# Optimization experiments

Measured on AMD Instinct MI355X. Metric: run time of the kernel, lower is better.

Reference implementation:

```python
import jax, jax.numpy as jnp
import numpy as np

B, T = 32, 512
LATENT, COND, HIDDEN, OUT, E = 64, 448, 1024, 512, 8
INPUT = LATENT + COND            # 512
INTER = LATENT + COND + HIDDEN   # 1536
GATE_H = 64


def setup_inputs() -> dict:
    key = jax.random.key(0)
    ks = jax.random.split(key, 20)
    d = {
        "z": jax.random.normal(ks[0], (B, T, LATENT), dtype=jnp.float32),
        "c": jax.random.normal(ks[1], (B, T, COND), dtype=jnp.float32),
    }
    # expert weights: kaiming-uniform-ish init, biases filled with 0.01 (as in torch code)
    layer_dims = [(INPUT, HIDDEN), (INTER, HIDDEN), (INTER, HIDDEN), (INTER, HIDDEN), (INTER, OUT)]
    for i, (fin, fout) in enumerate(layer_dims):
        bound = float(np.sqrt(6.0 / fin))
        d[f"w{i}"] = jax.random.uniform(ks[2 + i], (E, fin, fout), dtype=jnp.float32, minval=-bound, maxval=bound)
        d[f"b{i}"] = jnp.full((E, fout), 0.01, dtype=jnp.float32)
    # gate MLP: input_size -> 64 -> 64 -> E (stored as [in, out])
    gate_dims = [(INPUT, GATE_H), (GATE_H, GATE_H), (GATE_H, E)]
    for i, (fin, fout) in enumerate(gate_dims):
        bound = float(np.sqrt(1.0 / fin))
        d[f"gw{i}"] = jax.random.uniform(ks[10 + 2 * i], (fin, fout), dtype=jnp.float32, minval=-bound, maxval=bound)
        d[f"gb{i}"] = jax.random.uniform(ks[11 + 2 * i], (fout,), dtype=jnp.float32, minval=-bound, maxval=bound)
    return d


def reference(z, c, w0, b0, w1, b1, w2, b2, w3, b3, w4, b4, gw0, gb0, gw1, gb1, gw2, gb2):
    # gate -> per-token softmax mixing coefficients  [B, T, E]
    x = jnp.concatenate([z, c], axis=-1)
    h = jax.nn.leaky_relu(x @ gw0 + gb0)
    h = jax.nn.leaky_relu(h @ gw1 + gb1)
    coef = jax.nn.softmax(h @ gw2 + gb2, axis=-1)
    # Original computes mixed_weight for every t but baddbmm uses only mixed_weight[:, 0];
    # so the effective per-sequence weight uses coefficients at t=0 only (same math, no huge intermediate).
    coef0 = coef[:, 0]  # [B, E]
    layer_out = c
    layers = [(w0, b0, True), (w1, b1, True), (w2, b2, True), (w3, b3, True), (w4, b4, False)]
    for i, (w, b, act) in enumerate(layers):
        if i == 0:
            inp = jnp.concatenate([z, layer_out], axis=-1)      # [B, T, INPUT]
        else:
            inp = jnp.concatenate([z, c, layer_out], axis=-1)   # [B, T, INTER]
        wm = jnp.einsum('be,eio->bio', coef0, w)                # per-sequence mixed weight
        bm = jnp.einsum('bte,eo->bto', coef, b)                 # per-token mixed bias
        out = bm + jnp.einsum('bti,bio->bto', inp, wm)
        layer_out = jax.nn.leaky_relu(out) if act else out
    return layer_out
```

## Files before the change

### kernel.cpp

```cpp
#include <hip/hip_runtime.h>
#include <math.h>

#define B_     32
#define T_     512
#define LATENT 64
#define COND   448
#define HIDDEN 1024
#define OUTD   512
#define E_     8
#define INPUT_ 512
#define INTER_ 1536
#define GATEH  64
#define NTOK   (B_ * T_)
#define KTAIL  32

typedef __attribute__((ext_vector_type(8))) short short8;
typedef __attribute__((ext_vector_type(4))) float f32x4;

static __device__ __forceinline__ unsigned short f2bf(float x) {
    unsigned u = __float_as_uint(x);
    u += 0x7fffu + ((u >> 16) & 1u);
    return (unsigned short)(u >> 16);
}

__global__ __launch_bounds__(256) void wprep_kernel(
    const float* __restrict__ gw0, const float* __restrict__ gw1,
    unsigned short* __restrict__ gw0T, unsigned short* __restrict__ gw1T)
{
    int idx = blockIdx.x * 256 + threadIdx.x;
    if (idx < GATEH * INPUT_) {
        int n = idx >> 9, k = idx & 511;
        gw0T[n * INPUT_ + k] = f2bf(gw0[k * GATEH + n]);
    } else {
        int i2 = idx - GATEH * INPUT_;
        if (i2 < GATEH * GATEH) {
            int n = i2 >> 6, k = i2 & 63;
            gw1T[n * GATEH + k] = f2bf(gw1[k * GATEH + n]);
        }
    }
}

__global__ __launch_bounds__(256) void gate_kernel(
    const float* __restrict__ z, const float* __restrict__ c,
    const float* __restrict__ gb0,
    const float* __restrict__ gb1,
    const float* __restrict__ gw2, const float* __restrict__ gb2,
    const unsigned short* __restrict__ gw0T,
    const unsigned short* __restrict__ gw1T,
    float* __restrict__ coef, unsigned short* __restrict__ coefpad,
    unsigned short* __restrict__ xzb)
{
    __shared__ unsigned short Hb[GATEH][72];
    __shared__ float H2[GATEH][65];
    __shared__ float sLg[GATEH][E_];

    const int tid = threadIdx.x;
    const int lane = tid & 63;
    const int wv = tid >> 6;
    const int tok0 = blockIdx.x * 64;

#pragma unroll
    for (int i = 0; i < 4; ++i) {
        int idx = i * 256 + tid;
        int tr = idx >> 4, c4 = (idx & 15) * 4;
        float4 v = *(const float4*)(z + ((size_t)(tok0 + tr) * LATENT) + c4);
        ushort4 o = {f2bf(v.x), f2bf(v.y), f2bf(v.z), f2bf(v.w)};
        *(ushort4*)(xzb + (size_t)(tok0 + tr) * INPUT_ + c4) = o;
    }
#pragma unroll
    for (int i = 0; i < 28; ++i) {
        int idx = i * 256 + tid;
        int tr = idx / 112, c4 = (idx % 112) * 4;
        float4 v = *(const float4*)(c + ((size_t)(tok0 + tr) * COND) + c4);
        ushort4 o = {f2bf(v.x), f2bf(v.y), f2bf(v.z), f2bf(v.w)};
        *(ushort4*)(xzb + (size_t)(tok0 + tr) * INPUT_ + LATENT + c4) = o;
    }
    __threadfence_block();
    __syncthreads();

    const int fr = lane & 15, fq = lane >> 4;
    const int wm0 = (wv & 1) * 32, wn0 = (wv >> 1) * 32;

    f32x4 acc[2][2];
#pragma unroll
    for (int im = 0; im < 2; ++im)
#pragma unroll
        for (int in = 0; in < 2; ++in) acc[im][in] = (f32x4){0.f,0.f,0.f,0.f};

    for (int k0 = 0; k0 < INPUT_; k0 += 32) {
        short8 af[2], bf[2];
#pragma unroll
        for (int im = 0; im < 2; ++im)
            af[im] = *(const short8*)(xzb + (size_t)(tok0 + wm0 + im*16 + fr) * INPUT_
                                          + k0 + fq * 8);
#pragma unroll
        for (int in = 0; in < 2; ++in)
            bf[in] = *(const short8*)(gw0T + (size_t)(wn0 + in*16 + fr) * INPUT_
                                           + k0 + fq * 8);
#pragma unroll
        for (int im = 0; im < 2; ++im)
#pragma unroll
            for (int in = 0; in < 2; ++in)
                acc[im][in] = __builtin_amdgcn_mfma_f32_16x16x32_bf16(
                    af[im], bf[in], acc[im][in], 0, 0, 0);
    }
#pragma unroll
    for (int im = 0; im < 2; ++im)
#pragma unroll
        for (int in = 0; in < 2; ++in)
#pragma unroll
            for (int reg = 0; reg < 4; ++reg) {
                int m = wm0 + im*16 + fq*4 + reg;
                int n = wn0 + in*16 + fr;
                float h = acc[im][in][reg] + gb0[n];
                h = h > 0.f ? h : 0.01f * h;
                Hb[m][n] = f2bf(h);
            }
    __syncthreads();

    f32x4 a2[2][2];
#pragma unroll
    for (int im = 0; im < 2; ++im)
#pragma unroll
        for (int in = 0; in < 2; ++in) a2[im][in] = (f32x4){0.f,0.f,0.f,0.f};
#pragma unroll
    for (int k0 = 0; k0 < GATEH; k0 += 32) {
        short8 af[2], bf[2];
#pragma unroll
        for (int im = 0; im < 2; ++im)
            af[im] = *(const short8*)(&Hb[wm0 + im*16 + fr][k0 + fq*8]);
#pragma unroll
        for (int in = 0; in < 2; ++in)
            bf[in] = *(const short8*)(gw1T + (size_t)(wn0 + in*16 + fr) * GATEH
                                           + k0 + fq * 8);
#pragma unroll
        for (int im = 0; im < 2; ++im)
#pragma unroll
            for (int in = 0; in < 2; ++in)
                a2[im][in] = __builtin_amdgcn_mfma_f32_16x16x32_bf16(
                    af[im], bf[in], a2[im][in], 0, 0, 0);
    }
#pragma unroll
    for (int im = 0; im < 2; ++im)
#pragma unroll
        for (int in = 0; in < 2; ++in)
#pragma unroll
            for (int reg = 0; reg < 4; ++reg) {
                int m = wm0 + im*16 + fq*4 + reg;
                int n = wn0 + in*16 + fr;
                float h = a2[im][in][reg] + gb1[n];
                H2[m][n] = h > 0.f ? h : 0.01f * h;
            }
    __syncthreads();

    {
        int tok = tid >> 2, e0 = (tid & 3) * 2;
        float l0 = gb2[e0], l1 = gb2[e0 + 1];
#pragma unroll
        for (int i = 0; i < GATEH; ++i) {
            float h = H2[tok][i];
            l0 = fmaf(h, gw2[i * E_ + e0], l0);
            l1 = fmaf(h, gw2[i * E_ + e0 + 1], l1);
        }
        sLg[tok][e0] = l0; sLg[tok][e0 + 1] = l1;
    }
    __syncthreads();

    if (tid < 64) {
        int token = tok0 + tid;
        float lg[E_], m = -1e30f, s = 0.f;
#pragma unroll
        for (int e = 0; e < E_; ++e) { lg[e] = sLg[tid][e]; m = fmaxf(m, lg[e]); }
#pragma unroll
        for (int e = 0; e < E_; ++e) { lg[e] = expf(lg[e] - m); s += lg[e]; }
        float inv = 1.f / s;
        unsigned short pad[KTAIL];
#pragma unroll
        for (int e = 0; e < E_; ++e) {
            float cv = lg[e] * inv;
            coef[(size_t)token * E_ + e] = cv;
            pad[e] = f2bf(cv);
        }
#pragma unroll
        for (int j = E_; j < KTAIL; ++j) pad[j] = 0;
#pragma unroll
        for (int q = 0; q < 4; ++q)
            *(ushort4*)(coefpad + (size_t)token * KTAIL + q * 4) =
                *(const ushort4*)&pad[q * 4];
    }
}

#define MI 32
#define MO 64
#define MP 65

__global__ __launch_bounds__(256) void mixT_kernel(
    const float* __restrict__ w,
    const float* __restrict__ bias,
    const float* __restrict__ coef,
    unsigned short* __restrict__ wmT,
    int fin, int fout, int gb, int batch0)
{
    __shared__ float sW[E_][MI][MP];
    __shared__ float sC[B_][E_];
    const int t = threadIdx.x;
    const int fin_tot = fin + KTAIL;
    const int nbi = fin / MI;
    const int i0 = (blockIdx.x % nbi) * MI;
    const int o0 = (blockIdx.x / nbi) * MO;

    if (t < gb * E_)
        sC[t >> 3][t & 7] = coef[(size_t)(batch0 + (t >> 3)) * T_ * E_ + (t & 7)];

#pragma unroll
    for (int r = 0; r < 64; ++r) {
        int idx = r * 256 + t;
        int o = idx & 63;
        int i = (idx >> 6) & 31;
        int e = idx >> 11;
        sW[e][i][o] = w[(size_t)e * fin * fout + (size_t)(i0 + i) * fout + o0 + o];
    }
    __syncthreads();

    const int o  = t >> 2;
    const int i8 = (t & 3) * 8;
    for (int b = 0; b < gb; ++b) {
        float v[8];
#pragma unroll
        for (int j = 0; j < 8; ++j) v[j] = 0.f;
#pragma unroll
        for (int e = 0; e < E_; ++e) {
            float cc = sC[b][e];
#pragma unroll
            for (int j = 0; j < 8; ++j)
                v[j] = fmaf(cc, sW[e][i8 + j][o], v[j]);
        }
        unsigned short u[8];
#pragma unroll
        for (int j = 0; j < 8; ++j) u[j] = f2bf(v[j]);
        *(int4*)(wmT + ((size_t)b * fout + o0 + o) * fin_tot + i0 + i8) = *(const int4*)u;
    }

    if (i0 == 0) {
        const int jj = t & 3;
        unsigned short u[8];
#pragma unroll
        for (int q = 0; q < 8; ++q)
            u[q] = (jj == 0) ? f2bf(bias[(size_t)q * fout + o0 + o]) : 0;
        for (int b = 0; b < gb; ++b)
            *(int4*)(wmT + ((size_t)b * fout + o0 + o) * fin_tot + fin + jj * 8) =
                *(const int4*)u;
    }
}

__global__ __launch_bounds__(512, 2) void gemm_kernel(
    const unsigned short* __restrict__ xz,
    const unsigned short* __restrict__ prev,
    const unsigned short* __restrict__ wmT,
    const unsigned short* __restrict__ coefpad,
    float* __restrict__ outf,
    unsigned short* __restrict__ outb,
    int fin_tot, int fout, int act, int batch0)
{
    __shared__ __align__(16) unsigned short As[4][8192];
    __shared__ __align__(16) unsigned short Bs[4][8192];

    const int tid = threadIdx.x;
    const int lane = tid & 63;
    const int w8 = tid >> 6;
    const int wm = w8 & 1;
    const int wn = w8 >> 1;

    const int nx = gridDim.x;
    int bx = blockIdx.x, by = blockIdx.y, bz = blockIdx.z;
    {
        int nwg = nx * 2 * gridDim.z;
        if ((nwg & 7) == 0) {
            int f = blockIdx.x + nx * (blockIdx.y + 2 * blockIdx.z);
            int q = nwg >> 3;
            int wk = (f & 7) * q + (f >> 3);
            int bpb = nx * 2;
            bz = wk / bpb;
            int r = wk - bz * bpb;
            by = r / nx;
            bx = r - by * nx;
        }
    }

    const int row0 = by * 256;
    const int col0 = bx * 256;
    const size_t tokbase = (size_t)(batch0 + bz) * T_;
    const unsigned short* wmb = wmT + (size_t)bz * fin_tot * fout;

    const int lrow = lane >> 2;
    const int lk8  = (((lane & 3) ^ ((lane >> 3) & 3)) * 8);
    const int fr = lane & 15, fq = lane >> 4;
    const int koff = (fq ^ ((fr >> 1) & 3)) * 8;
    const int ktail0 = fin_tot - KTAIL;
    const int nt = fin_tot >> 5;

    f32x4 acc[8][4];
#pragma unroll
    for (int im = 0; im < 8; ++im)
#pragma unroll
        for (int in = 0; in < 4; ++in)
            acc[im][in] = (f32x4){0.f, 0.f, 0.f, 0.f};

    auto stage = [&](int t) {
        int k0 = t << 5;
        const unsigned short* abase; int astr, acol;
        if (k0 < INPUT_)      { abase = xz;      astr = INPUT_; acol = k0; }
        else if (k0 < ktail0) { abase = prev;    astr = HIDDEN; acol = k0 - INPUT_; }
        else                  { abase = coefpad; astr = KTAIL;  acol = 0; }
        unsigned short* Ab = As[t & 3];
        unsigned short* Bb = Bs[t & 3];
#pragma unroll
        for (int j = 0; j < 2; ++j) {
            int ch = w8 + 8 * j;
            const unsigned short* srcA = abase
                + (tokbase + row0 + ch * 16 + lrow) * (size_t)astr + acol + lk8;
            __builtin_amdgcn_global_load_lds(
                (const __attribute__((address_space(1))) unsigned int*)(const void*)srcA,
                (__attribute__((address_space(3))) unsigned int*)(void*)(Ab + ch * 512),
                16, 0, 0);
            const unsigned short* srcB = wmb
                + (size_t)(col0 + ch * 16 + lrow) * fin_tot + k0 + lk8;
            __builtin_amdgcn_global_load_lds(
                (const __attribute__((address_space(1))) unsigned int*)(const void*)srcB,
                (__attribute__((address_space(3))) unsigned int*)(void*)(Bb + ch * 512),
                16, 0, 0);
        }
    };

    stage(0);
    if (nt > 1) stage(1);
    if (nt > 2) stage(2);

    for (int t = 0; t < nt; ++t) {
        int rem = nt - 1 - t;
        if (rem >= 2)
            asm volatile("s_waitcnt vmcnt(8)\n\ts_barrier" ::: "memory");
        else if (rem == 1)
            asm volatile("s_waitcnt vmcnt(4)\n\ts_barrier" ::: "memory");
        else
            asm volatile("s_waitcnt vmcnt(0)\n\ts_barrier" ::: "memory");

        if (t + 3 < nt) stage(t + 3);

        const unsigned short* Ab = As[t & 3] + wm * 4096;
        const unsigned short* Bb = Bs[t & 3] + wn * 2048;
        short8 af[8], bfv[4];
#pragma unroll
        for (int im = 0; im < 8; ++im)
            af[im] = *(const short8*)(Ab + im * 512 + fr * 32 + koff);
#pragma unroll
        for (int in = 0; in < 4; ++in)
            bfv[in] = *(const short8*)(Bb + in * 512 + fr * 32 + koff);

        __builtin_amdgcn_s_setprio(1);
#pragma unroll
        for (int im = 0; im < 8; ++im)
#pragma unroll
            for (int in = 0; in < 4; ++in)
                acc[im][in] = __builtin_amdgcn_mfma_f32_16x16x32_bf16(
                    af[im], bfv[in], acc[im][in], 0, 0, 0);
        __builtin_amdgcn_s_setprio(0);
    }

#pragma unroll
    for (int im = 0; im < 8; ++im) {
#pragma unroll
        for (int in = 0; in < 4; ++in) {
#pragma unroll
            for (int reg = 0; reg < 4; ++reg) {
                int r = wm * 128 + im * 16 + fq * 4 + reg;
                int col = wn * 64 + in * 16 + fr;
                float v = acc[im][in][reg];
                if (act) v = v > 0.f ? v : 0.01f * v;
                size_t off = (tokbase + row0 + r) * fout + col0 + col;
                if (outb) outb[off] = f2bf(v);
                else      outf[off] = v;
            }
        }
    }
}

extern "C" void kernel_launch(void* const* d_in, const int* in_sizes, int n_in,
                              void* d_out, int out_size, void* d_ws, size_t ws_size,
                              hipStream_t stream)
{
    const float* z = (const float*)d_in[0];
    const float* c = (const float*)d_in[1];
    const float* w[5]  = {(const float*)d_in[2], (const float*)d_in[4],
                          (const float*)d_in[6], (const float*)d_in[8],
                          (const float*)d_in[10]};
    const float* bs[5] = {(const float*)d_in[3], (const float*)d_in[5],
                          (const float*)d_in[7], (const float*)d_in[9],
                          (const float*)d_in[11]};
    const float* gw0 = (const float*)d_in[12]; const float* gb0 = (const float*)d_in[13];
    const float* gw1 = (const float*)d_in[14]; const float* gb1 = (const float*)d_in[15];
    const float* gw2 = (const float*)d_in[16]; const float* gb2 = (const float*)d_in[17];

    const size_t g0t_b  = (size_t)GATEH * INPUT_ * 2;
    const size_t g1t_b  = (size_t)GATEH * GATEH * 2;
    const size_t xz_b   = (size_t)NTOK * INPUT_ * 2;
    const size_t coef_b = (size_t)NTOK * E_ * 4;
    const size_t cpad_b = (size_t)NTOK * KTAIL * 2;
    const size_t act_b  = (size_t)NTOK * HIDDEN * 2;
    const size_t wmun   = (size_t)(INTER_ + KTAIL) * HIDDEN * 2;

    char* p = (char*)d_ws;
    unsigned short* gw0T  = (unsigned short*)p;  p += g0t_b;
    unsigned short* gw1T  = (unsigned short*)p;  p += g1t_b;
    unsigned short* xzb   = (unsigned short*)p;  p += xz_b;
    float*          coef  = (float*)p;           p += coef_b;
    unsigned short* cpad  = (unsigned short*)p;  p += cpad_b;
    unsigned short* actB  = (unsigned short*)p;  p += act_b;

    size_t base = g0t_b + g1t_b + xz_b + coef_b + cpad_b + act_b;
    size_t avail = (ws_size > base) ? ws_size - base : 0;

    int gb;
    unsigned short* actA;
    unsigned short* wmT;
    if (avail >= act_b + 32 * wmun) {
        gb = 32; actA = (unsigned short*)p; p += act_b; wmT = (unsigned short*)p;
    } else {
        actA = (unsigned short*)d_out;
        wmT  = (unsigned short*)p;
        gb = 1;
        for (int g = 16; g >= 2; g >>= 1)
            if (avail >= (size_t)g * wmun) { gb = g; break; }
    }

    wprep_kernel<<<(GATEH * (INPUT_ + GATEH) + 255) / 256, 256, 0, stream>>>(
        gw0, gw1, gw0T, gw1T);
    gate_kernel<<<NTOK / 64, 256, 0, stream>>>(
        z, c, gb0, gb1, gw2, gb2, gw0T, gw1T, coef, cpad, xzb);

    struct L { int fin, fout, act; const unsigned short* in; unsigned short* outb; };
    L Ls[5] = {
        {INPUT_, HIDDEN, 1, actB , actA},
        {INTER_, HIDDEN, 1, actA, actB},
        {INTER_, HIDDEN, 1, actB, actA},
        {INTER_, HIDDEN, 1, actA, actB},
        {INTER_, OUTD,   0, actB, 0},
    };

    for (int Li = 0; Li < 5; ++Li) {
        int fin = Ls[Li].fin, fout = Ls[Li].fout;
        int nblk = (fin / MI) * (fout / MO);
        for (int g = 0; g < B_; g += gb) {
            mixT_kernel<<<nblk, 256, 0, stream>>>(
                w[Li], bs[Li], coef, wmT, fin, fout, gb, g);
            gemm_kernel<<<dim3(fout / 256, T_ / 256, gb), 512, 0, stream>>>(
                xzb, Ls[Li].in, wmT, cpad,
                (float*)d_out, Ls[Li].outb, fin + KTAIL, fout, Ls[Li].act, g);
        }
    }
}
```

Measured before the change: 698.4 us.

## Restructure GEMM main loop into BK=64 ping-pong schedule with interleaved staging

Doubles the K step per iteration to 64, switching from a 4-deep ring of 32-wide stages to a double-buffered pair of 64-wide stages. Each iteration is split into four quarter-phases that interleave global-to-LDS loads for the next tile with LDS reads and MFMA clusters, separated by barriers. The coefficient/bias tail is padded to 64 columns so K stays a multiple of 64, adding extra zero K work and more barriers. The aim is better overlap of memory and MFMA with fewer outer iterations, at the cost of a shallower prefetch depth.

```diff
diff --git a/kernel.cpp b/kernel.cpp
--- a/kernel.cpp
+++ b/kernel.cpp
@@ -12,7 +12,7 @@
 #define INTER_ 1536
 #define GATEH  64
 #define NTOK   (B_ * T_)
-#define KTAIL  32
+#define KTAIL  64
 
 typedef __attribute__((ext_vector_type(8))) short short8;
 typedef __attribute__((ext_vector_type(4))) float f32x4;
@@ -184,7 +184,7 @@
 #pragma unroll
         for (int j = E_; j < KTAIL; ++j) pad[j] = 0;
 #pragma unroll
-        for (int q = 0; q < 4; ++q)
+        for (int q = 0; q < KTAIL / 4; ++q)
             *(ushort4*)(coefpad + (size_t)token * KTAIL + q * 4) =
                 *(const ushort4*)&pad[q * 4];
     }
@@ -247,9 +247,12 @@
 #pragma unroll
         for (int q = 0; q < 8; ++q)
             u[q] = (jj == 0) ? f2bf(bias[(size_t)q * fout + o0 + o]) : 0;
-        for (int b = 0; b < gb; ++b)
-            *(int4*)(wmT + ((size_t)b * fout + o0 + o) * fin_tot + fin + jj * 8) =
-                *(const int4*)u;
+        unsigned short z8[8] = {0, 0, 0, 0, 0, 0, 0, 0};
+        for (int b = 0; b < gb; ++b) {
+            size_t rb = ((size_t)b * fout + o0 + o) * fin_tot + fin;
+            *(int4*)(wmT + rb + jj * 8)      = *(const int4*)u;
+            *(int4*)(wmT + rb + 32 + jj * 8) = *(const int4*)z8;
+        }
     }
 }
 
@@ -262,8 +265,8 @@
     unsigned short* __restrict__ outb,
     int fin_tot, int fout, int act, int batch0)
 {
-    __shared__ __align__(16) unsigned short As[4][8192];
-    __shared__ __align__(16) unsigned short Bs[4][8192];
+    __shared__ __align__(16) unsigned short As[2][2][8192];
+    __shared__ __align__(16) unsigned short Bs[2][2][8192];
 
     const int tid = threadIdx.x;
     const int lane = tid & 63;
@@ -297,7 +300,7 @@
     const int fr = lane & 15, fq = lane >> 4;
     const int koff = (fq ^ ((fr >> 1) & 3)) * 8;
     const int ktail0 = fin_tot - KTAIL;
-    const int nt = fin_tot >> 5;
+    const int nt = fin_tot >> 6;
 
     f32x4 acc[8][4];
 #pragma unroll
@@ -306,64 +309,144 @@
         for (int in = 0; in < 4; ++in)
             acc[im][in] = (f32x4){0.f, 0.f, 0.f, 0.f};
 
-    auto stage = [&](int t) {
-        int k0 = t << 5;
+    auto stageA = [&](int t, int kk) {
+        int k32 = (t << 6) + (kk << 5);
         const unsigned short* abase; int astr, acol;
-        if (k0 < INPUT_)      { abase = xz;      astr = INPUT_; acol = k0; }
-        else if (k0 < ktail0) { abase = prev;    astr = HIDDEN; acol = k0 - INPUT_; }
-        else                  { abase = coefpad; astr = KTAIL;  acol = 0; }
-        unsigned short* Ab = As[t & 3];
-        unsigned short* Bb = Bs[t & 3];
+        if (k32 < INPUT_)      { abase = xz;      astr = INPUT_; acol = k32; }
+        else if (k32 < ktail0) { abase = prev;    astr = HIDDEN; acol = k32 - INPUT_; }
+        else                   { abase = coefpad; astr = KTAIL;  acol = k32 - ktail0; }
+        unsigned short* Ab = &As[t & 1][kk][0];
 #pragma unroll
         for (int j = 0; j < 2; ++j) {
             int ch = w8 + 8 * j;
-            const unsigned short* srcA = abase
+            const unsigned short* src = abase
                 + (tokbase + row0 + ch * 16 + lrow) * (size_t)astr + acol + lk8;
             __builtin_amdgcn_global_load_lds(
-                (const __attribute__((address_space(1))) unsigned int*)(const void*)srcA,
+                (const __attribute__((address_space(1))) unsigned int*)(const void*)src,
                 (__attribute__((address_space(3))) unsigned int*)(void*)(Ab + ch * 512),
                 16, 0, 0);
-            const unsigned short* srcB = wmb
-                + (size_t)(col0 + ch * 16 + lrow) * fin_tot + k0 + lk8;
+        }
+    };
+    auto stageB = [&](int t, int kk) {
+        int k32 = (t << 6) + (kk << 5);
+        unsigned short* Bb = &Bs[t & 1][kk][0];
+#pragma unroll
+        for (int j = 0; j < 2; ++j) {
+            int ch = w8 + 8 * j;
+            const unsigned short* src = wmb
+                + (size_t)(col0 + ch * 16 + lrow) * fin_tot + k32 + lk8;
             __builtin_amdgcn_global_load_lds(
-                (const __attribute__((address_space(1))) unsigned int*)(const void*)srcB,
+                (const __attribute__((address_space(1))) unsigned int*)(const void*)src,
                 (__attribute__((address_space(3))) unsigned int*)(void*)(Bb + ch * 512),
                 16, 0, 0);
         }
     };
 
-    stage(0);
-    if (nt > 1) stage(1);
-    if (nt > 2) stage(2);
-
-    for (int t = 0; t < nt; ++t) {
-        int rem = nt - 1 - t;
-        if (rem >= 2)
-            asm volatile("s_waitcnt vmcnt(8)\n\ts_barrier" ::: "memory");
-        else if (rem == 1)
-            asm volatile("s_waitcnt vmcnt(4)\n\ts_barrier" ::: "memory");
-        else
-            asm volatile("s_waitcnt vmcnt(0)\n\ts_barrier" ::: "memory");
-
-        if (t + 3 < nt) stage(t + 3);
-
-        const unsigned short* Ab = As[t & 3] + wm * 4096;
-        const unsigned short* Bb = Bs[t & 3] + wn * 2048;
-        short8 af[8], bfv[4];
-#pragma unroll
-        for (int im = 0; im < 8; ++im)
-            af[im] = *(const short8*)(Ab + im * 512 + fr * 32 + koff);
-#pragma unroll
-        for (int in = 0; in < 4; ++in)
-            bfv[in] = *(const short8*)(Bb + in * 512 + fr * 32 + koff);
-
-        __builtin_amdgcn_s_setprio(1);
-#pragma unroll
-        for (int im = 0; im < 8; ++im)
+    auto readA4 = [&](const unsigned short* Ak, int im0, short8* af) {
+#pragma unroll
+        for (int q = 0; q < 4; ++q)
+            af[q] = *(const short8*)(Ak + (im0 + q) * 512 + fr * 32 + koff);
+    };
+    auto readB4 = [&](const unsigned short* Bk, short8* bv) {
+#pragma unroll
+        for (int q = 0; q < 4; ++q)
+            bv[q] = *(const short8*)(Bk + q * 512 + fr * 32 + koff);
+    };
+    auto mfma16 = [&](int im0, short8* af, short8* bv) {
+#pragma unroll
+        for (int q = 0; q < 4; ++q)
 #pragma unroll
             for (int in = 0; in < 4; ++in)
-                acc[im][in] = __builtin_amdgcn_mfma_f32_16x16x32_bf16(
-                    af[im], bfv[in], acc[im][in], 0, 0, 0);
+                acc[im0 + q][in] = __builtin_amdgcn_mfma_f32_16x16x32_bf16(
+                    af[q], bv[in], acc[im0 + q][in], 0, 0, 0);
+    };
+
+    stageA(0, 0); stageB(0, 0); stageA(0, 1); stageB(0, 1);
+    asm volatile("s_waitcnt vmcnt(4)" ::: "memory");
+    __builtin_amdgcn_s_barrier();
+
+    for (int t = 0; t < nt - 1; ++t) {
+        const int cur = t & 1;
+        const unsigned short* A0  = &As[cur][0][wm * 4096];
+        const unsigned short* A1  = &As[cur][1][wm * 4096];
+        const unsigned short* Bk0 = &Bs[cur][0][wn * 2048];
+        const unsigned short* Bk1 = &Bs[cur][1][wn * 2048];
+        short8 af[4], bv[4];
+
+        readA4(A0, 0, af); readB4(Bk0, bv);
+        stageA(t + 1, 0);
+        __builtin_amdgcn_s_barrier();
+        asm volatile("s_waitcnt lgkmcnt(0)" ::: "memory");
+        __builtin_amdgcn_s_setprio(1);
+        mfma16(0, af, bv);
+        __builtin_amdgcn_s_setprio(0);
+        __builtin_amdgcn_s_barrier();
+
+        readA4(A0, 4, af);
+        stageB(t + 1, 0);
+        asm volatile("s_waitcnt vmcnt(4)" ::: "memory");
+        __builtin_amdgcn_s_barrier();
+        asm volatile("s_waitcnt lgkmcnt(0)" ::: "memory");
+        __builtin_amdgcn_s_setprio(1);
+        mfma16(4, af, bv);
+        __builtin_amdgcn_s_setprio(0);
+        __builtin_amdgcn_s_barrier();
+
+        readA4(A1, 0, af); readB4(Bk1, bv);
+        stageA(t + 1, 1);
+        __builtin_amdgcn_s_barrier();
+        asm volatile("s_waitcnt lgkmcnt(0)" ::: "memory");
+        __builtin_amdgcn_s_setprio(1);
+        mfma16(0, af, bv);
+        __builtin_amdgcn_s_setprio(0);
+        __builtin_amdgcn_s_barrier();
+
+        readA4(A1, 4, af);
+        stageB(t + 1, 1);
+        asm volatile("s_waitcnt vmcnt(4)" ::: "memory");
+        __builtin_amdgcn_s_barrier();
+        asm volatile("s_waitcnt lgkmcnt(0)" ::: "memory");
+        __builtin_amdgcn_s_setprio(1);
+        mfma16(4, af, bv);
+        __builtin_amdgcn_s_setprio(0);
+        __builtin_amdgcn_s_barrier();
+    }
+
+    {
+        const int cur = (nt - 1) & 1;
+        const unsigned short* A0  = &As[cur][0][wm * 4096];
+        const unsigned short* A1  = &As[cur][1][wm * 4096];
+        const unsigned short* Bk0 = &Bs[cur][0][wn * 2048];
+        const unsigned short* Bk1 = &Bs[cur][1][wn * 2048];
+        short8 af[4], bv[4];
+
+        readA4(A0, 0, af); readB4(Bk0, bv);
+        __builtin_amdgcn_s_barrier();
+        asm volatile("s_waitcnt lgkmcnt(0)" ::: "memory");
+        __builtin_amdgcn_s_setprio(1);
+        mfma16(0, af, bv);
+        __builtin_amdgcn_s_setprio(0);
+        __builtin_amdgcn_s_barrier();
+
+        readA4(A0, 4, af);
+        asm volatile("s_waitcnt vmcnt(0)" ::: "memory");
+        __builtin_amdgcn_s_barrier();
+        asm volatile("s_waitcnt lgkmcnt(0)" ::: "memory");
+        __builtin_amdgcn_s_setprio(1);
+        mfma16(4, af, bv);
+        __builtin_amdgcn_s_setprio(0);
+        __builtin_amdgcn_s_barrier();
+
+        readA4(A1, 0, af); readB4(Bk1, bv);
+        asm volatile("s_waitcnt lgkmcnt(0)" ::: "memory");
+        __builtin_amdgcn_s_setprio(1);
+        mfma16(0, af, bv);
+        __builtin_amdgcn_s_setprio(0);
+
+        readA4(A1, 4, af);
+        asm volatile("s_waitcnt lgkmcnt(0)" ::: "memory");
+        __builtin_amdgcn_s_setprio(1);
+        mfma16(4, af, bv);
         __builtin_amdgcn_s_setprio(0);
     }
 
```

Result: no change. 685.1 us (-1.9%).
